# Performance work log

Hardware: AMD Instinct MI355X
Metric: run time of the kernel (lower is better)

Reference implementation:

```python
import jax, jax.numpy as jnp
import numpy as np

EPS = 1e-6
NUM_HEADS = 16

def _rms(x, w=None):
    y = x * jax.lax.rsqrt(jnp.mean(x * x, axis=-1, keepdims=True) + EPS)
    return y if w is None else y * w

def _rope(q, k, pos):
    # q,k: [B,H,T,Dh]; half-split (rotate_half) RoPE convention, base 10000
    dh = q.shape[-1]
    half = dh // 2
    freqs = 1.0 / (10000.0 ** (jnp.arange(half, dtype=jnp.float32) / half))
    ang = pos.astype(jnp.float32)[:, None] * freqs[None, :]  # [T, half]
    cos = jnp.concatenate([jnp.cos(ang), jnp.cos(ang)], -1)  # [T, Dh]
    sin = jnp.concatenate([jnp.sin(ang), jnp.sin(ang)], -1)
    def rot(v):
        v1, v2 = jnp.split(v, 2, axis=-1)
        return jnp.concatenate([-v2, v1], -1)
    return q * cos + rot(q) * sin, k * cos + rot(k) * sin


def setup_inputs() -> dict:
    key = jax.random.key(0)
    ks = jax.random.split(key, 12)
    B, T, D, H = 2, 2048, 1024, NUM_HEADS
    Dh = D // H
    Hm = 2816  # SwiGLU hidden: multiple_of*ceil(int(2*4*D/3)/256)
    s = lambda fan_in: 1.0 / np.sqrt(fan_in)
    return {
        "x": jax.random.normal(ks[0], (B, T, D), jnp.float32),
        "c": jax.random.normal(ks[1], (B, D), jnp.float32),
        "pos": jnp.arange(T, dtype=jnp.int32),
        "adaln_w": jax.random.normal(ks[2], (D, 6 * D), jnp.float32) * s(D) * 0.1,
        "adaln_b": jax.random.normal(ks[3], (6 * D,), jnp.float32) * 0.02,
        "qkv_w": jax.random.normal(ks[4], (D, 3 * D), jnp.float32) * s(D),
        "lnq_w": jnp.ones((Dh,), jnp.float32),
        "lnk_w": jnp.ones((Dh,), jnp.float32),
        "proj_w": jax.random.normal(ks[5], (D, D), jnp.float32) * s(D),
        "proj_b": jnp.zeros((D,), jnp.float32),
        "w1_w": jax.random.normal(ks[6], (D, Hm), jnp.float32) * s(D),
        "w3_w": jax.random.normal(ks[7], (D, Hm), jnp.float32) * s(D),
        "w2_w": jax.random.normal(ks[8], (Hm, D), jnp.float32) * s(Hm),
    }


def reference(x, c, pos, adaln_w, adaln_b, qkv_w, lnq_w, lnk_w, proj_w, proj_b, w1_w, w3_w, w2_w):
    B, T, D = x.shape
    H = NUM_HEADS
    Dh = D // H

    # AdaLN: SiLU -> Linear -> chunk(6)
    mods = jax.nn.silu(c) @ adaln_w + adaln_b  # [B,6D]
    shift_msa, scale_msa, gate_msa, shift_mlp, scale_mlp, gate_mlp = jnp.split(mods, 6, axis=-1)

    # norm1 (RMSNorm, no affine) + modulate along seq dim
    x_mod = _rms(x) * (1.0 + scale_msa[:, None, :]) + shift_msa[:, None, :]

    # QKV projection (no bias)
    qkv = x_mod @ qkv_w  # [B,T,3D]
    q, k, v = jnp.split(qkv, 3, axis=-1)
    q = q.reshape(B, T, H, Dh).transpose(0, 2, 1, 3)  # [B,H,T,Dh]
    k = k.reshape(B, T, H, Dh).transpose(0, 2, 1, 3)
    v = v.reshape(B, T, H, Dh).transpose(0, 2, 1, 3)

    # per-head RMS qk-norm with affine weight
    q = _rms(q, lnq_w)
    k = _rms(k, lnk_w)

    # 1D RoPE
    q, k = _rope(q, k, pos)

    # attention core (SDPA, delegated in the original module)
    scores = jnp.einsum('bhqd,bhkd->bhqk', q, k) / jnp.sqrt(jnp.float32(Dh))
    attn = jax.nn.softmax(scores, axis=-1)
    attn_out = jnp.einsum('bhqk,bhkd->bhqd', attn, v)  # [B,H,T,Dh]
    attn_out = attn_out.transpose(0, 2, 1, 3).reshape(B, T, D)

    # post_attention: gated residual + SwiGLU MLP
    x = x + gate_msa[:, None, :] * (attn_out @ proj_w + proj_b)
    h = _rms(x) * (1.0 + scale_mlp[:, None, :]) + shift_mlp[:, None, :]
    mlp = (jax.nn.silu(h @ w1_w) * (h @ w3_w)) @ w2_w
    x = x + gate_mlp[:, None, :] * mlp
    return x
```

## Files before the change

kernel.cpp:

```cpp
#include <hip/hip_runtime.h>
#include <stdint.h>
#include <math.h>

typedef unsigned short u16;
typedef __attribute__((ext_vector_type(4))) float f32x4;
typedef __attribute__((ext_vector_type(16))) float f32x16;
typedef __attribute__((ext_vector_type(8))) __bf16 bf16x8;

#define DEV static __device__ __forceinline__

typedef __attribute__((address_space(1))) void gvoid;
typedef __attribute__((address_space(3))) void lvoid;

DEV float bf2f(u16 u){ uint32_t v = ((uint32_t)u) << 16; float f; __builtin_memcpy(&f, &v, 4); return f; }
DEV u16 f2bf(float f){ uint32_t v; __builtin_memcpy(&v, &f, 4); v = (v + 0x7fffu + ((v >> 16) & 1u)) >> 16; return (u16)v; }

DEV void cp16(const void* g, void* l){
  __builtin_amdgcn_global_load_lds((gvoid*)g, (lvoid*)l, 16, 0, 0);
}
DEV f32x4 mfma16(bf16x8 a, bf16x8 b, f32x4 c){
  return __builtin_amdgcn_mfma_f32_16x16x32_bf16(a, b, c, 0, 0, 0);
}
DEV f32x16 mfma32(bf16x8 a, bf16x8 b, f32x16 c){
  return __builtin_amdgcn_mfma_f32_32x32x16_bf16(a, b, c, 0, 0, 0);
}
DEV uint32_t cvtpk(float a, float b){
  uint32_t r;
  asm volatile("v_cvt_pk_bf16_f32 %0, %1, %2" : "=v"(r) : "v"(a), "v"(b));
  return r;
}
DEV void uswap(uint32_t& a, uint32_t& b){
  asm volatile("v_permlane32_swap_b32 %0, %1" : "+v"(a), "+v"(b));
}
DEV void fswap(float& a, float& b){
  asm volatile("v_permlane32_swap_b32 %0, %1" : "+v"(a), "+v"(b));
}
DEV float fexp2(float x){
  float r;
  asm("v_exp_f32 %0, %1" : "=v"(r) : "v"(x));
  return r;
}

__global__ void __launch_bounds__(256) adaln1(const float* __restrict__ c,
                                              const float* __restrict__ w,
                                              float* __restrict__ part)
{
  __shared__ float sc[256];
  int k0 = blockIdx.y * 128;
  {
    int i = threadIdx.x;
    int b = i >> 7, kk = i & 127;
    float v = c[b * 1024 + k0 + kk];
    sc[i] = v / (1.f + __expf(-v));
  }
  __syncthreads();
  int col = blockIdx.x * 256 + threadIdx.x;
  float a0 = 0.f, a1 = 0.f;
  #pragma unroll 8
  for (int k = 0; k < 128; ++k){
    float wv = w[(size_t)(k0 + k) * 6144 + col];
    a0 += sc[k] * wv;
    a1 += sc[128 + k] * wv;
  }
  part[((size_t)blockIdx.y * 2 + 0) * 6144 + col] = a0;
  part[((size_t)blockIdx.y * 2 + 1) * 6144 + col] = a1;
}

__global__ void __launch_bounds__(256) adaln2(const float* __restrict__ part,
                                              const float* __restrict__ bias,
                                              float* __restrict__ mods)
{
  int i = blockIdx.x * 256 + threadIdx.x;
  int b = i / 6144, col = i % 6144;
  float a = bias[col];
  #pragma unroll
  for (int r = 0; r < 8; ++r) a += part[((size_t)r * 2 + b) * 6144 + col];
  mods[i] = a;
}

__global__ void __launch_bounds__(256) rope_table(const int* __restrict__ pos,
                                                  float* __restrict__ ct,
                                                  float* __restrict__ st)
{
  int idx = blockIdx.x * 256 + threadIdx.x;
  int t = idx >> 5, i = idx & 31;
  float freq = expf(-0.28782313662425575f * (float)i);
  float ang = (float)pos[t] * freq;
  ct[idx] = cosf(ang);
  st[idx] = sinf(ang);
}

__global__ void __launch_bounds__(256) rmsmod(const float* __restrict__ x,
                                              const float* __restrict__ mods,
                                              u16* __restrict__ out,
                                              int shift_off, int scale_off)
{
  __shared__ float wsum[4];
  int row = blockIdx.x;
  int b = row >> 11;
  const float4 v = ((const float4*)(x + (size_t)row * 1024))[threadIdx.x];
  float ss = v.x * v.x + v.y * v.y + v.z * v.z + v.w * v.w;
  #pragma unroll
  for (int m = 1; m < 64; m <<= 1) ss += __shfl_xor(ss, m);
  if ((threadIdx.x & 63) == 0) wsum[threadIdx.x >> 6] = ss;
  __syncthreads();
  float tot = wsum[0] + wsum[1] + wsum[2] + wsum[3];
  float rr = rsqrtf(tot * (1.f / 1024.f) + 1e-6f);
  const float* mb = mods + (size_t)b * 6144;
  int d0 = threadIdx.x * 4;
  ushort4 o;
  o.x = f2bf(v.x * rr * (1.f + mb[scale_off + d0 + 0]) + mb[shift_off + d0 + 0]);
  o.y = f2bf(v.y * rr * (1.f + mb[scale_off + d0 + 1]) + mb[shift_off + d0 + 1]);
  o.z = f2bf(v.z * rr * (1.f + mb[scale_off + d0 + 2]) + mb[shift_off + d0 + 2]);
  o.w = f2bf(v.w * rr * (1.f + mb[scale_off + d0 + 3]) + mb[shift_off + d0 + 3]);
  ((ushort4*)(out + (size_t)row * 1024))[threadIdx.x] = o;
}

__global__ void __launch_bounds__(256) transpose_w(const float* __restrict__ in,
                                                   u16* __restrict__ out, int R, int C)
{
  __shared__ float t[32][33];
  int tx = threadIdx.x & 31, ty = threadIdx.x >> 5;
  int c0 = blockIdx.x * 32, r0 = blockIdx.y * 32;
  #pragma unroll
  for (int i = 0; i < 4; ++i) t[ty + 8 * i][tx] = in[(size_t)(r0 + ty + 8 * i) * C + c0 + tx];
  __syncthreads();
  #pragma unroll
  for (int i = 0; i < 4; ++i) out[(size_t)(c0 + ty + 8 * i) * R + r0 + tx] = f2bf(t[tx][ty + 8 * i]);
}

__global__ void __launch_bounds__(256) vtrans(const u16* __restrict__ qkv,
                                              u16* __restrict__ vt)
{
  __shared__ u16 tile[32][33];
  int tx = threadIdx.x & 31, ty = threadIdx.x >> 5;
  int t0 = blockIdx.x * 32;
  int d0 = blockIdx.y * 32;
  int bh = blockIdx.z; int b = bh >> 4, h = bh & 15;
  #pragma unroll
  for (int i = 0; i < 4; ++i) {
    int t = t0 + ty + 8 * i;
    tile[ty + 8 * i][tx] = qkv[((size_t)(b * 2048 + t)) * 3072 + 2048 + h * 64 + d0 + tx];
  }
  __syncthreads();
  #pragma unroll
  for (int i = 0; i < 4; ++i) {
    int d = d0 + ty + 8 * i;
    vt[((size_t)bh * 64 + d) * 2048 + t0 + tx] = tile[tx][ty + 8 * i];
  }
}

template<int EPI>
__global__ void __launch_bounds__(256) gemm_bt(const u16* __restrict__ A,
                                               const u16* __restrict__ Bt,
                                               int M, int N, int K,
                                               const float* __restrict__ mods, int gate_off,
                                               const float* __restrict__ bias,
                                               const float* __restrict__ res,
                                               const u16* __restrict__ aux,
                                               float* __restrict__ outf,
                                               u16* __restrict__ outb)
{
  __shared__ __align__(16) u16 Ash[128 * 64];
  __shared__ __align__(16) u16 Bsh[128 * 64];
  const int tid = threadIdx.x;
  const int l = tid & 63, w = tid >> 6;
  const int nwg = gridDim.x * gridDim.y;
  const int id = blockIdx.y * gridDim.x + blockIdx.x;
  const int nid = (id & 7) * (nwg >> 3) + (id >> 3);
  const int bx = nid % gridDim.x, by = nid / gridDim.x;
  const int m0 = by * 128, n0 = bx * 128;
  const int wr = (w >> 1) * 64, wc = (w & 1) * 64;
  const int fr = l & 15, fg = l >> 4;
  const int sw = fr & 7;
  f32x4 acc[4][4] = {};

  for (int kt = 0; kt < K; kt += 64) {
    __syncthreads();
    #pragma unroll
    for (int p = 0; p < 4; ++p) {
      int slot = p * 256 + tid;
      int r = slot >> 3, kp = slot & 7;
      int kpg = kp ^ (r & 7);
      cp16(A + (size_t)(m0 + r) * K + kt + kpg * 8, Ash + slot * 8);
      cp16(Bt + (size_t)(n0 + r) * K + kt + kpg * 8, Bsh + slot * 8);
    }
    __syncthreads();
    #pragma unroll
    for (int kk = 0; kk < 2; ++kk) {
      const int coff = ((kk * 4 + fg) ^ sw) * 8;
      bf16x8 af[4], bfr[4];
      #pragma unroll
      for (int m = 0; m < 4; ++m) af[m] = *(const bf16x8*)(Ash + (wr + m * 16 + fr) * 64 + coff);
      #pragma unroll
      for (int n = 0; n < 4; ++n) bfr[n] = *(const bf16x8*)(Bsh + (wc + n * 16 + fr) * 64 + coff);
      #pragma unroll
      for (int m = 0; m < 4; ++m)
        #pragma unroll
        for (int n = 0; n < 4; ++n)
          acc[m][n] = mfma16(af[m], bfr[n], acc[m][n]);
    }
  }

  #pragma unroll
  for (int m = 0; m < 4; ++m)
  #pragma unroll
  for (int n = 0; n < 4; ++n)
  #pragma unroll
  for (int j = 0; j < 4; ++j) {
    int row = m0 + wr + m * 16 + fg * 4 + j;
    int col = n0 + wc + n * 16 + fr;
    size_t idx = (size_t)row * N + col;
    float v = acc[m][n][j];
    if (EPI == 0) {
      outb[idx] = f2bf(v);
    } else if (EPI == 1) {
      int b = row >> 11;
      outf[idx] = res[idx] + mods[(size_t)b * 6144 + gate_off + col] * (v + bias[col]);
    } else if (EPI == 2) {
      outb[idx] = f2bf(v / (1.f + __expf(-v)));
    } else if (EPI == 3) {
      outb[idx] = f2bf(bf2f(aux[idx]) * v);
    } else {
      int b = row >> 11;
      outf[idx] = res[idx] + mods[(size_t)b * 6144 + gate_off + col] * v;
    }
  }
}

__global__ void __launch_bounds__(256) qknorm_rope(const u16* __restrict__ qkv,
                                                   const float* __restrict__ lnq,
                                                   const float* __restrict__ lnk,
                                                   const float* __restrict__ ctab,
                                                   const float* __restrict__ stab,
                                                   u16* __restrict__ qo,
                                                   u16* __restrict__ ko)
{
  int r = blockIdx.x * 4 + (threadIdx.x >> 6);
  int l = threadIdx.x & 63;
  int h = r & 15, t = (r >> 4) & 2047, b = r >> 15;
  const u16* base = qkv + ((size_t)(b * 2048 + t)) * 3072 + h * 64 + l;
  float q = bf2f(base[0]);
  float k = bf2f(base[1024]);
  float sq = q * q, sk = k * k;
  #pragma unroll
  for (int m = 1; m < 64; m <<= 1) { sq += __shfl_xor(sq, m); sk += __shfl_xor(sk, m); }
  float rq = rsqrtf(sq * (1.f / 64.f) + 1e-6f);
  float rk = rsqrtf(sk * (1.f / 64.f) + 1e-6f);
  float yq = q * rq * lnq[l];
  float yk = k * rk * lnk[l];
  float cs = ctab[t * 32 + (l & 31)];
  float sn = stab[t * 32 + (l & 31)];
  float pq = __shfl_xor(yq, 32);
  float pk = __shfl_xor(yk, 32);
  float rotq = (l < 32) ? -pq : pq;
  float rotk = (l < 32) ? -pk : pk;
  float oq = (yq * cs + rotq * sn) * 0.1803368801111204f;
  float ok = yk * cs + rotk * sn;
  size_t oidx = ((size_t)(b * 16 + h) * 2048 + t) * 64 + l;
  qo[oidx] = f2bf(oq);
  ko[oidx] = f2bf(ok);
}

__global__ void __launch_bounds__(256, 2) flash_attn(const u16* __restrict__ qg,
                                                     const u16* __restrict__ kg,
                                                     const u16* __restrict__ vtg,
                                                     u16* __restrict__ og)
{
  __shared__ __align__(16) char smem[65536];
  const int tid = threadIdx.x, l = tid & 63, w = tid >> 6;
  const int lq = l & 31, hi = l >> 5;
  const int swz = lq & 7;
  const int xcd = blockIdx.x & 7, slot = blockIdx.x >> 3;
  const int g = slot >> 4, qt = slot & 15;
  const int bh = g * 8 + xcd;
  const int h = bh & 15, b = bh >> 4;

  bf16x8 qf[4];
  {
    const u16* qp = qg + ((size_t)bh * 2048 + qt * 128 + w * 32 + lq) * 64 + hi * 8;
    #pragma unroll
    for (int ks = 0; ks < 4; ++ks) qf[ks] = *(const bf16x8*)(qp + ks * 16);
  }
  const u16* kgb = kg + (size_t)bh * 2048 * 64;
  const u16* vgb = vtg + (size_t)bh * 64 * 2048;

  auto stage = [&](int kv, int bsel) {
    #pragma unroll
    for (int p = 0; p < 4; ++p) {
      int s2 = p * 256 + tid;
      int r = s2 >> 3, cl = s2 & 7;
      int cg = cl ^ (r & 7);
      cp16(kgb + (size_t)(kv + r) * 64 + cg * 8, smem + bsel * 16384 + s2 * 16);
    }
    #pragma unroll
    for (int p = 0; p < 4; ++p) {
      int s2 = p * 256 + tid;
      int r = s2 >> 4, cl = s2 & 15;
      int cg = cl ^ (r & 7);
      cp16(vgb + (size_t)r * 2048 + kv + cg * 8, smem + 32768 + bsel * 16384 + s2 * 16);
    }
  };

  f32x16 ob0 = {}, ob1 = {};
  float l_run = 0.f;

  stage(0, 0);
  __syncthreads();

  for (int t = 0; t < 16; ++t) {
    const int cur = t & 1;
    stage(((t + 1) & 15) * 128, cur ^ 1);
    const char* Kb = smem + cur * 16384;
    const char* Vb = smem + 32768 + cur * 16384;

    #pragma unroll
    for (int ko = 0; ko < 128; ko += 64) {
      f32x16 s0 = {}, s1 = {};
      __builtin_amdgcn_s_setprio(1);
      #pragma unroll
      for (int ks = 0; ks < 4; ++ks) {
        const int c = hi + ks * 2;
        bf16x8 kf0 = *(const bf16x8*)(Kb + (ko + lq) * 128 + ((c ^ swz) << 4));
        bf16x8 kf1 = *(const bf16x8*)(Kb + (ko + 32 + lq) * 128 + ((c ^ swz) << 4));
        s0 = mfma32(kf0, qf[ks], s0);
        s1 = mfma32(kf1, qf[ks], s1);
      }
      __builtin_amdgcn_s_setprio(0);
      #pragma unroll
      for (int r = 0; r < 16; ++r) s0[r] = fexp2(s0[r]);
      #pragma unroll
      for (int r = 0; r < 16; ++r) s1[r] = fexp2(s1[r]);
      {
        float t0 = (s0[0] + s0[1]) + (s0[2] + s0[3]);
        float t1 = (s0[4] + s0[5]) + (s0[6] + s0[7]);
        float t2 = (s0[8] + s0[9]) + (s0[10] + s0[11]);
        float t3 = (s0[12] + s0[13]) + (s0[14] + s0[15]);
        float u0 = (s1[0] + s1[1]) + (s1[2] + s1[3]);
        float u1 = (s1[4] + s1[5]) + (s1[6] + s1[7]);
        float u2 = (s1[8] + s1[9]) + (s1[10] + s1[11]);
        float u3 = (s1[12] + s1[13]) + (s1[14] + s1[15]);
        float ls = ((t0 + t1) + (t2 + t3)) + ((u0 + u1) + (u2 + u3));
        float lo = ls;
        fswap(ls, lo);
        l_run += ls + lo;
      }
      uint32_t pw[16];
      {
        uint32_t x0 = cvtpk(s0[0], s0[1]),   y0 = cvtpk(s0[4], s0[5]);   uswap(x0, y0);
        uint32_t x1 = cvtpk(s0[2], s0[3]),   y1 = cvtpk(s0[6], s0[7]);   uswap(x1, y1);
        uint32_t x2 = cvtpk(s0[8], s0[9]),   y2 = cvtpk(s0[12], s0[13]); uswap(x2, y2);
        uint32_t x3 = cvtpk(s0[10], s0[11]), y3 = cvtpk(s0[14], s0[15]); uswap(x3, y3);
        pw[0] = x0; pw[1] = x1; pw[2] = y0; pw[3] = y1;
        pw[4] = x2; pw[5] = x3; pw[6] = y2; pw[7] = y3;
      }
      {
        uint32_t x0 = cvtpk(s1[0], s1[1]),   y0 = cvtpk(s1[4], s1[5]);   uswap(x0, y0);
        uint32_t x1 = cvtpk(s1[2], s1[3]),   y1 = cvtpk(s1[6], s1[7]);   uswap(x1, y1);
        uint32_t x2 = cvtpk(s1[8], s1[9]),   y2 = cvtpk(s1[12], s1[13]); uswap(x2, y2);
        uint32_t x3 = cvtpk(s1[10], s1[11]), y3 = cvtpk(s1[14], s1[15]); uswap(x3, y3);
        pw[8] = x0;  pw[9] = x1;  pw[10] = y0; pw[11] = y1;
        pw[12] = x2; pw[13] = x3; pw[14] = y2; pw[15] = y3;
      }
      __builtin_amdgcn_s_setprio(1);
      #pragma unroll
      for (int ks = 0; ks < 4; ++ks) {
        union { uint32_t u[4]; bf16x8 v; } pk_;
        pk_.u[0] = pw[ks * 4 + 0]; pk_.u[1] = pw[ks * 4 + 1];
        pk_.u[2] = pw[ks * 4 + 2]; pk_.u[3] = pw[ks * 4 + 3];
        const int c = (ko >> 3) + ks * 2 + hi;
        bf16x8 vf0 = *(const bf16x8*)(Vb + lq * 256 + ((c ^ swz) << 4));
        bf16x8 vf1 = *(const bf16x8*)(Vb + (32 + lq) * 256 + ((c ^ swz) << 4));
        ob0 = mfma32(vf0, pk_.v, ob0);
        ob1 = mfma32(vf1, pk_.v, ob1);
      }
      __builtin_amdgcn_s_setprio(0);
    }
    __syncthreads();
  }

  float invl = 1.0f / l_run;
  char* ob_base = smem + w * 4096 + lq * 128 + 8 * hi;
  #pragma unroll
  for (int g2 = 0; g2 < 4; ++g2) {
    uint2 t2;
    t2.x = cvtpk(ob0[g2 * 4 + 0] * invl, ob0[g2 * 4 + 1] * invl);
    t2.y = cvtpk(ob0[g2 * 4 + 2] * invl, ob0[g2 * 4 + 3] * invl);
    *(uint2*)(ob_base + ((g2 ^ (lq & 7)) << 4)) = t2;
    uint2 t3;
    t3.x = cvtpk(ob1[g2 * 4 + 0] * invl, ob1[g2 * 4 + 1] * invl);
    t3.y = cvtpk(ob1[g2 * 4 + 2] * invl, ob1[g2 * 4 + 3] * invl);
    *(uint2*)(ob_base + (((g2 + 4) ^ (lq & 7)) << 4)) = t3;
  }
  __syncthreads();
  #pragma unroll
  for (int i = 0; i < 4; ++i) {
    int idx = i * 256 + tid;
    int ww = idx >> 8, q = (idx >> 3) & 31, s = idx & 7;
    uint4 val = *(const uint4*)(smem + ww * 4096 + q * 128 + ((s ^ (q & 7)) << 4));
    int t = qt * 128 + ww * 32 + q;
    *(uint4*)(og + ((size_t)(b * 2048 + t)) * 1024 + h * 64 + s * 8) = val;
  }
}

extern "C" void kernel_launch(void* const* d_in, const int* in_sizes, int n_in,
                              void* d_out, int out_size, void* d_ws, size_t ws_size,
                              hipStream_t stream)
{
  (void)in_sizes; (void)n_in; (void)out_size; (void)ws_size;
  const float* x       = (const float*)d_in[0];
  const float* c       = (const float*)d_in[1];
  const int*   pos     = (const int*)d_in[2];
  const float* adaln_w = (const float*)d_in[3];
  const float* adaln_b = (const float*)d_in[4];
  const float* qkv_w   = (const float*)d_in[5];
  const float* lnq     = (const float*)d_in[6];
  const float* lnk     = (const float*)d_in[7];
  const float* proj_w  = (const float*)d_in[8];
  const float* proj_b  = (const float*)d_in[9];
  const float* w1_w    = (const float*)d_in[10];
  const float* w3_w    = (const float*)d_in[11];
  const float* w2_w    = (const float*)d_in[12];
  float* out = (float*)d_out;

  char* ws = (char*)d_ws;
  size_t off = 0;
  auto alloc = [&](size_t bytes) -> char* {
    char* p = ws + off; off += (bytes + 255) & ~(size_t)255; return p;
  };
  float* part    = (float*)alloc((size_t)8 * 2 * 6144 * 4);
  float* mods    = (float*)alloc((size_t)2 * 6144 * 4);
  float* ctab    = (float*)alloc((size_t)2048 * 32 * 4);
  float* stab    = (float*)alloc((size_t)2048 * 32 * 4);
  u16* qkv_wt    = (u16*)alloc((size_t)3072 * 1024 * 2);
  u16* proj_wt   = (u16*)alloc((size_t)1024 * 1024 * 2);
  u16* w1_wt     = (u16*)alloc((size_t)2816 * 1024 * 2);
  u16* w3_wt     = (u16*)alloc((size_t)2816 * 1024 * 2);
  u16* w2_wt     = (u16*)alloc((size_t)1024 * 2816 * 2);
  float* x1      = (float*)alloc((size_t)4096 * 1024 * 4);
  u16* attn_bf   = (u16*)alloc((size_t)4096 * 1024 * 2);
  char* pool = ws + off;
  u16* xmod_bf   = (u16*)(pool);
  u16* qkv_bf    = (u16*)(pool + 8388608);
  u16* q_bf      = (u16*)(pool + 33554432);
  u16* k_bf      = (u16*)(pool + 41943040);
  u16* vt_bf     = (u16*)(pool + 50331648);
  u16* h_bf      = (u16*)(pool);
  u16* t1_bf     = (u16*)(pool + 8388608);
  u16* hidden_bf = (u16*)(pool + 31457280);

  adaln1<<<dim3(24, 8), 256, 0, stream>>>(c, adaln_w, part);
  adaln2<<<48, 256, 0, stream>>>(part, adaln_b, mods);
  rope_table<<<256, 256, 0, stream>>>(pos, ctab, stab);
  rmsmod<<<4096, 256, 0, stream>>>(x, mods, xmod_bf, 0, 1024);
  transpose_w<<<dim3(96, 32), 256, 0, stream>>>(qkv_w, qkv_wt, 1024, 3072);
  transpose_w<<<dim3(32, 32), 256, 0, stream>>>(proj_w, proj_wt, 1024, 1024);
  transpose_w<<<dim3(88, 32), 256, 0, stream>>>(w1_w, w1_wt, 1024, 2816);
  transpose_w<<<dim3(88, 32), 256, 0, stream>>>(w3_w, w3_wt, 1024, 2816);
  transpose_w<<<dim3(32, 88), 256, 0, stream>>>(w2_w, w2_wt, 2816, 1024);

  gemm_bt<0><<<dim3(24, 32), 256, 0, stream>>>(xmod_bf, qkv_wt, 4096, 3072, 1024,
                                               nullptr, 0, nullptr, nullptr, nullptr,
                                               nullptr, qkv_bf);
  qknorm_rope<<<16384, 256, 0, stream>>>(qkv_bf, lnq, lnk, ctab, stab, q_bf, k_bf);
  vtrans<<<dim3(64, 2, 32), 256, 0, stream>>>(qkv_bf, vt_bf);
  flash_attn<<<512, 256, 0, stream>>>(q_bf, k_bf, vt_bf, attn_bf);
  gemm_bt<1><<<dim3(8, 32), 256, 0, stream>>>(attn_bf, proj_wt, 4096, 1024, 1024,
                                              mods, 2048, proj_b, x, nullptr,
                                              x1, nullptr);
  rmsmod<<<4096, 256, 0, stream>>>(x1, mods, h_bf, 3072, 4096);
  gemm_bt<2><<<dim3(22, 32), 256, 0, stream>>>(h_bf, w1_wt, 4096, 2816, 1024,
                                               nullptr, 0, nullptr, nullptr, nullptr,
                                               nullptr, t1_bf);
  gemm_bt<3><<<dim3(22, 32), 256, 0, stream>>>(h_bf, w3_wt, 4096, 2816, 1024,
                                               nullptr, 0, nullptr, nullptr, t1_bf,
                                               nullptr, hidden_bf);
  gemm_bt<4><<<dim3(8, 32), 256, 0, stream>>>(hidden_bf, w2_wt, 4096, 1024, 2816,
                                              mods, 5120, nullptr, x1, nullptr,
                                              out, nullptr);
}
```

Baseline: 288.7 us.

## Fuse W1/W3 SwiGLU GEMMs and add double-buffered skinny GEMM for N=1024

```diff
diff --git a/kernel.cpp b/kernel.cpp
--- a/kernel.cpp
+++ b/kernel.cpp
@@ -150,15 +150,9 @@
   }
 }
 
-template<int EPI>
 __global__ void __launch_bounds__(256) gemm_bt(const u16* __restrict__ A,
                                                const u16* __restrict__ Bt,
                                                int M, int N, int K,
-                                               const float* __restrict__ mods, int gate_off,
-                                               const float* __restrict__ bias,
-                                               const float* __restrict__ res,
-                                               const u16* __restrict__ aux,
-                                               float* __restrict__ outf,
                                                u16* __restrict__ outb)
 {
   __shared__ __align__(16) u16 Ash[128 * 64];
@@ -210,21 +204,166 @@
   for (int j = 0; j < 4; ++j) {
     int row = m0 + wr + m * 16 + fg * 4 + j;
     int col = n0 + wc + n * 16 + fr;
+    outb[(size_t)row * N + col] = f2bf(acc[m][n][j]);
+  }
+}
+
+template<int EPI>
+__global__ void __launch_bounds__(256) gemm_skinny(const u16* __restrict__ A,
+                                                   const u16* __restrict__ Bt,
+                                                   int M, int N, int K,
+                                                   const float* __restrict__ mods,
+                                                   int gate_off,
+                                                   const float* __restrict__ bias,
+                                                   const float* __restrict__ res,
+                                                   float* __restrict__ outf)
+{
+  __shared__ __align__(16) u16 Ash[2][64 * 64];
+  __shared__ __align__(16) u16 Bsh[2][128 * 64];
+  const int tid = threadIdx.x;
+  const int l = tid & 63, w = tid >> 6;
+  const int nwg = gridDim.x * gridDim.y;
+  const int id = blockIdx.y * gridDim.x + blockIdx.x;
+  const int nid = (id & 7) * (nwg >> 3) + (id >> 3);
+  const int bx = nid % gridDim.x, by = nid / gridDim.x;
+  const int m0 = by * 64, n0 = bx * 128;
+  const int wr = (w >> 1) * 32, wc = (w & 1) * 64;
+  const int fr = l & 15, fg = l >> 4;
+  const int sw = fr & 7;
+  const int nk = K >> 6;
+  f32x4 acc[2][4] = {};
+
+  auto stage = [&](int kt, int bsel) {
+    #pragma unroll
+    for (int p = 0; p < 2; ++p) {
+      int slot = p * 256 + tid;
+      int r = slot >> 3, kp = slot & 7;
+      int kpg = kp ^ (r & 7);
+      cp16(A + (size_t)(m0 + r) * K + kt + kpg * 8, &Ash[bsel][slot * 8]);
+    }
+    #pragma unroll
+    for (int p = 0; p < 4; ++p) {
+      int slot = p * 256 + tid;
+      int r = slot >> 3, kp = slot & 7;
+      int kpg = kp ^ (r & 7);
+      cp16(Bt + (size_t)(n0 + r) * K + kt + kpg * 8, &Bsh[bsel][slot * 8]);
+    }
+  };
+
+  stage(0, 0);
+  __syncthreads();
+
+  for (int t = 0; t < nk; ++t) {
+    if (t + 1 < nk) stage((t + 1) << 6, (t + 1) & 1);
+    const u16* Ab = Ash[t & 1];
+    const u16* Bb = Bsh[t & 1];
+    #pragma unroll
+    for (int kk = 0; kk < 2; ++kk) {
+      const int coff = ((kk * 4 + fg) ^ sw) * 8;
+      bf16x8 af[2], bfr[4];
+      #pragma unroll
+      for (int m = 0; m < 2; ++m) af[m] = *(const bf16x8*)(Ab + (wr + m * 16 + fr) * 64 + coff);
+      #pragma unroll
+      for (int n = 0; n < 4; ++n) bfr[n] = *(const bf16x8*)(Bb + (wc + n * 16 + fr) * 64 + coff);
+      #pragma unroll
+      for (int m = 0; m < 2; ++m)
+        #pragma unroll
+        for (int n = 0; n < 4; ++n)
+          acc[m][n] = mfma16(af[m], bfr[n], acc[m][n]);
+    }
+    __syncthreads();
+  }
+
+  #pragma unroll
+  for (int m = 0; m < 2; ++m)
+  #pragma unroll
+  for (int n = 0; n < 4; ++n)
+  #pragma unroll
+  for (int j = 0; j < 4; ++j) {
+    int row = m0 + wr + m * 16 + fg * 4 + j;
+    int col = n0 + wc + n * 16 + fr;
     size_t idx = (size_t)row * N + col;
     float v = acc[m][n][j];
-    if (EPI == 0) {
-      outb[idx] = f2bf(v);
-    } else if (EPI == 1) {
-      int b = row >> 11;
+    int b = row >> 11;
+    if (EPI == 1)
       outf[idx] = res[idx] + mods[(size_t)b * 6144 + gate_off + col] * (v + bias[col]);
-    } else if (EPI == 2) {
-      outb[idx] = f2bf(v / (1.f + __expf(-v)));
-    } else if (EPI == 3) {
-      outb[idx] = f2bf(bf2f(aux[idx]) * v);
-    } else {
-      int b = row >> 11;
+    else
       outf[idx] = res[idx] + mods[(size_t)b * 6144 + gate_off + col] * v;
-    }
+  }
+}
+
+__global__ void __launch_bounds__(256) gemm_w13(const u16* __restrict__ A,
+                                                const u16* __restrict__ B1t,
+                                                const u16* __restrict__ B3t,
+                                                u16* __restrict__ outb)
+{
+  const int K = 1024, N = 2816;
+  __shared__ __align__(16) u16 Ash[128 * 64];
+  __shared__ __align__(16) u16 B1sh[64 * 64];
+  __shared__ __align__(16) u16 B3sh[64 * 64];
+  const int tid = threadIdx.x;
+  const int l = tid & 63, w = tid >> 6;
+  const int nwg = gridDim.x * gridDim.y;
+  const int id = blockIdx.y * gridDim.x + blockIdx.x;
+  const int nid = (id & 7) * (nwg >> 3) + (id >> 3);
+  const int bx = nid % gridDim.x, by = nid / gridDim.x;
+  const int m0 = by * 128, n0 = bx * 64;
+  const int wr = (w >> 1) * 64, wc = (w & 1) * 32;
+  const int fr = l & 15, fg = l >> 4;
+  const int sw = fr & 7;
+  f32x4 acc1[4][2] = {}, acc3[4][2] = {};
+
+  for (int kt = 0; kt < K; kt += 64) {
+    __syncthreads();
+    #pragma unroll
+    for (int p = 0; p < 4; ++p) {
+      int slot = p * 256 + tid;
+      int r = slot >> 3, kp = slot & 7;
+      int kpg = kp ^ (r & 7);
+      cp16(A + (size_t)(m0 + r) * K + kt + kpg * 8, Ash + slot * 8);
+    }
+    #pragma unroll
+    for (int p = 0; p < 2; ++p) {
+      int slot = p * 256 + tid;
+      int r = slot >> 3, kp = slot & 7;
+      int kpg = kp ^ (r & 7);
+      cp16(B1t + (size_t)(n0 + r) * K + kt + kpg * 8, B1sh + slot * 8);
+      cp16(B3t + (size_t)(n0 + r) * K + kt + kpg * 8, B3sh + slot * 8);
+    }
+    __syncthreads();
+    #pragma unroll
+    for (int kk = 0; kk < 2; ++kk) {
+      const int coff = ((kk * 4 + fg) ^ sw) * 8;
+      bf16x8 af[4], b1f[2], b3f[2];
+      #pragma unroll
+      for (int m = 0; m < 4; ++m) af[m] = *(const bf16x8*)(Ash + (wr + m * 16 + fr) * 64 + coff);
+      #pragma unroll
+      for (int n = 0; n < 2; ++n) {
+        b1f[n] = *(const bf16x8*)(B1sh + (wc + n * 16 + fr) * 64 + coff);
+        b3f[n] = *(const bf16x8*)(B3sh + (wc + n * 16 + fr) * 64 + coff);
+      }
+      #pragma unroll
+      for (int m = 0; m < 4; ++m)
+        #pragma unroll
+        for (int n = 0; n < 2; ++n) {
+          acc1[m][n] = mfma16(af[m], b1f[n], acc1[m][n]);
+          acc3[m][n] = mfma16(af[m], b3f[n], acc3[m][n]);
+        }
+    }
+  }
+
+  #pragma unroll
+  for (int m = 0; m < 4; ++m)
+  #pragma unroll
+  for (int n = 0; n < 2; ++n)
+  #pragma unroll
+  for (int j = 0; j < 4; ++j) {
+    int row = m0 + wr + m * 16 + fg * 4 + j;
+    int col = n0 + wc + n * 16 + fr;
+    float v1 = acc1[m][n][j];
+    float v3 = acc3[m][n][j];
+    float s = v1 / (1.f + __expf(-v1));
+    outb[(size_t)row * N + col] = f2bf(s * v3);
   }
 }
 
@@ -446,7 +585,6 @@
   u16* k_bf      = (u16*)(pool + 41943040);
   u16* vt_bf     = (u16*)(pool + 50331648);
   u16* h_bf      = (u16*)(pool);
-  u16* t1_bf     = (u16*)(pool + 8388608);
   u16* hidden_bf = (u16*)(pool + 31457280);
 
   adaln1<<<dim3(24, 8), 256, 0, stream>>>(c, adaln_w, part);
@@ -459,23 +597,14 @@
   transpose_w<<<dim3(88, 32), 256, 0, stream>>>(w3_w, w3_wt, 1024, 2816);
   transpose_w<<<dim3(32, 88), 256, 0, stream>>>(w2_w, w2_wt, 2816, 1024);
 
-  gemm_bt<0><<<dim3(24, 32), 256, 0, stream>>>(xmod_bf, qkv_wt, 4096, 3072, 1024,
-                                               nullptr, 0, nullptr, nullptr, nullptr,
-                                               nullptr, qkv_bf);
+  gemm_bt<<<dim3(24, 32), 256, 0, stream>>>(xmod_bf, qkv_wt, 4096, 3072, 1024, qkv_bf);
   qknorm_rope<<<16384, 256, 0, stream>>>(qkv_bf, lnq, lnk, ctab, stab, q_bf, k_bf);
   vtrans<<<dim3(64, 2, 32), 256, 0, stream>>>(qkv_bf, vt_bf);
   flash_attn<<<512, 256, 0, stream>>>(q_bf, k_bf, vt_bf, attn_bf);
-  gemm_bt<1><<<dim3(8, 32), 256, 0, stream>>>(attn_bf, proj_wt, 4096, 1024, 1024,
-                                              mods, 2048, proj_b, x, nullptr,
-                                              x1, nullptr);
+  gemm_skinny<1><<<dim3(8, 64), 256, 0, stream>>>(attn_bf, proj_wt, 4096, 1024, 1024,
+                                                  mods, 2048, proj_b, x, x1);
   rmsmod<<<4096, 256, 0, stream>>>(x1, mods, h_bf, 3072, 4096);
-  gemm_bt<2><<<dim3(22, 32), 256, 0, stream>>>(h_bf, w1_wt, 4096, 2816, 1024,
-                                               nullptr, 0, nullptr, nullptr, nullptr,
-                                               nullptr, t1_bf);
-  gemm_bt<3><<<dim3(22, 32), 256, 0, stream>>>(h_bf, w3_wt, 4096, 2816, 1024,
-                                               nullptr, 0, nullptr, nullptr, t1_bf,
-                                               nullptr, hidden_bf);
-  gemm_bt<4><<<dim3(8, 32), 256, 0, stream>>>(hidden_bf, w2_wt, 4096, 1024, 2816,
-                                              mods, 5120, nullptr, x1, nullptr,
-                                              out, nullptr);
-}
+  gemm_w13<<<dim3(44, 32), 256, 0, stream>>>(h_bf, w1_wt, w3_wt, hidden_bf);
+  gemm_skinny<4><<<dim3(8, 64), 256, 0, stream>>>(hidden_bf, w2_wt, 4096, 1024, 2816,
+                                                  mods, 5120, nullptr, x1, out);
+}
```

Result: faster. 254.1 us (-12.0%).
